# Kernel optimization log

Hardware: AMD Instinct MI355X
Metric: run time of the kernel (lower is better)

Reference implementation:

```python
import jax, jax.numpy as jnp
import numpy as np

B, SQ, SK, D, H = 8, 1024, 1024, 768, 12
HD = D // H  # 64


def setup_inputs() -> dict:
    key = jax.random.key(0)
    ks = jax.random.split(key, 6)
    s = 0.02
    return {
        "hidden_states": jax.random.normal(ks[0], (B, SQ, D), jnp.float32),
        "context": jax.random.normal(ks[1], (B, SK, D), jnp.float32),
        "attention_mask": jnp.zeros((B, 1, 1, SK), jnp.float32),
        "Wq": jax.random.normal(ks[2], (D, D), jnp.float32) * s,
        "bq": jnp.zeros((D,), jnp.float32),
        "Wk": jax.random.normal(ks[3], (D, D), jnp.float32) * s,
        "bk": jnp.zeros((D,), jnp.float32),
        "Wv": jax.random.normal(ks[4], (D, D), jnp.float32) * s,
        "bv": jnp.zeros((D,), jnp.float32),
    }


def _split_heads(x):
    # [B, S, D] -> [B, H, S, HD]
    b, s, _ = x.shape
    return x.reshape(b, s, H, HD).transpose(0, 2, 1, 3)


def reference(hidden_states, context, attention_mask, Wq, bq, Wk, bk, Wv, bv):
    q = _split_heads(hidden_states @ Wq + bq)   # [B,H,SQ,HD]
    k = _split_heads(context @ Wk + bk)         # [B,H,SK,HD]
    v = _split_heads(context @ Wv + bv)         # [B,H,SK,HD]
    scores = jnp.einsum("bhqd,bhkd->bhqk", q, k) / jnp.sqrt(jnp.float32(HD))
    scores = scores + attention_mask            # broadcast [B,1,1,SK]
    probs = jax.nn.softmax(scores, axis=-1)     # dropout p=0 -> identity
    ctx = jnp.einsum("bhqk,bhkd->bhqd", probs, v)
    return ctx.transpose(0, 2, 1, 3).reshape(hidden_states.shape[0], -1, H * HD)
```

## Files before the change

### kernel.cpp

```cpp
#include <hip/hip_runtime.h>
#include <hip/hip_bf16.h>
#include <cstdint>

#define B_  8
#define SQ_ 1024
#define SK_ 1024
#define D_  768
#define H_  12
#define HD_ 64

typedef __attribute__((ext_vector_type(8))) short s16x8;
typedef __attribute__((ext_vector_type(4))) float f32x4;
typedef __attribute__((ext_vector_type(16))) float f32x16;

__device__ __forceinline__ float bf2f(ushort u) {
    union { uint32_t i; float f; } v; v.i = ((uint32_t)u) << 16; return v.f;
}
__device__ __forceinline__ ushort f2bf(float f) {
    __hip_bfloat16 h = __float2bfloat16(f);
    union { __hip_bfloat16 h; ushort u; } v; v.h = h; return v.u;
}
__device__ __forceinline__ uint32_t pk32(float a, float b) {
    return (uint32_t)f2bf(a) | ((uint32_t)f2bf(b) << 16);
}
__device__ __forceinline__ float fexp2(float x) {
#if __has_builtin(__builtin_amdgcn_exp2f)
    return __builtin_amdgcn_exp2f(x);
#else
    return exp2f(x);
#endif
}
__device__ __forceinline__ void xch(uint32_t a, uint32_t b, bool lo, uint32_t& x, uint32_t& y) {
    uint32_t bx = (uint32_t)__shfl_xor((int)b, 32);
    uint32_t ax = (uint32_t)__shfl_xor((int)a, 32);
    x = lo ? a : bx;
    y = lo ? ax : b;
}

__global__ void convX(const float4* __restrict__ src, ushort* __restrict__ dst, int n4) {
    int i = blockIdx.x * blockDim.x + threadIdx.x;
    int stride = gridDim.x * blockDim.x;
    for (; i < n4; i += stride) {
        float4 v = src[i];
        ushort4 o = { f2bf(v.x), f2bf(v.y), f2bf(v.z), f2bf(v.w) };
        *reinterpret_cast<ushort4*>(dst + (size_t)i * 4) = o;
    }
}

__global__ void convWT(const float* __restrict__ W, ushort* __restrict__ WT) {
    __shared__ float t[32][33];
    int k0 = blockIdx.x * 32, n0 = blockIdx.y * 32;
    int tx = threadIdx.x & 31, ty = threadIdx.x >> 5;
#pragma unroll
    for (int rr = 0; rr < 4; ++rr)
        t[ty + 8 * rr][tx] = W[(size_t)(k0 + ty + 8 * rr) * D_ + n0 + tx];
    __syncthreads();
#pragma unroll
    for (int rr = 0; rr < 4; ++rr)
        WT[(size_t)(n0 + ty + 8 * rr) * D_ + k0 + tx] = f2bf(t[tx][ty + 8 * rr]);
}

#define GL16(g, l)                                                                     \
    __builtin_amdgcn_global_load_lds((const __attribute__((address_space(1))) void*)(g), \
                                     (__attribute__((address_space(3))) void*)(l), 16, 0, 0)

__global__ __launch_bounds__(256) void gemm_qkv(
    const ushort* __restrict__ hb, const ushort* __restrict__ cb,
    const ushort* __restrict__ wqt, const ushort* __restrict__ wkt, const ushort* __restrict__ wvt,
    const float* __restrict__ bq, const float* __restrict__ bk, const float* __restrict__ bv,
    ushort* __restrict__ qout, ushort* __restrict__ kout, ushort* __restrict__ vtout)
{
    const int z = blockIdx.z;
    const ushort* A    = (z == 0) ? hb : cb;
    const ushort* Wt   = (z == 0) ? wqt : (z == 1) ? wkt : wvt;
    const float*  bias = (z == 0) ? bq  : (z == 1) ? bk  : bv;

    __shared__ ushort As[128 * 32];
    __shared__ ushort Bs[128 * 32];

    const int tid = threadIdx.x;
    const int w = tid >> 6, l = tid & 63;
    const int g = l >> 4, c = l & 15;
    const int wr = w >> 1, wc = w & 1;
    const int m0 = blockIdx.x * 128;
    const int n0 = blockIdx.y * 128;

    f32x4 acc[4][4];
#pragma unroll
    for (int mi = 0; mi < 4; ++mi)
#pragma unroll
        for (int ni = 0; ni < 4; ++ni) acc[mi][ni] = (f32x4){0.f, 0.f, 0.f, 0.f};

    for (int kt = 0; kt < D_ / 32; ++kt) {
        __syncthreads();
#pragma unroll
        for (int j = 0; j < 2; ++j) {
            int cc = (j * 4 + w) * 64 + l;
            int row = cc >> 2, c8 = cc & 3;
            const ushort* ga = A  + (size_t)(m0 + row) * D_ + kt * 32 + c8 * 8;
            GL16(ga, (char*)As + (size_t)(j * 4 + w) * 1024);
            const ushort* gb = Wt + (size_t)(n0 + row) * D_ + kt * 32 + c8 * 8;
            GL16(gb, (char*)Bs + (size_t)(j * 4 + w) * 1024);
        }
        __syncthreads();

        s16x8 af[4], bfr[4];
#pragma unroll
        for (int mi = 0; mi < 4; ++mi)
            af[mi] = *(const s16x8*)&As[(wr * 64 + mi * 16 + c) * 32 + g * 8];
#pragma unroll
        for (int ni = 0; ni < 4; ++ni)
            bfr[ni] = *(const s16x8*)&Bs[(wc * 64 + ni * 16 + c) * 32 + g * 8];
#pragma unroll
        for (int mi = 0; mi < 4; ++mi)
#pragma unroll
            for (int ni = 0; ni < 4; ++ni)
                acc[mi][ni] = __builtin_amdgcn_mfma_f32_16x16x32_bf16(af[mi], bfr[ni], acc[mi][ni], 0, 0, 0);
    }

    if (z < 2) {
        ushort* Out = (z == 0) ? qout : kout;
#pragma unroll
        for (int ni = 0; ni < 4; ++ni) {
            int ncol = n0 + wc * 64 + ni * 16 + c;
            float bv_ = bias[ncol];
#pragma unroll
            for (int mi = 0; mi < 4; ++mi) {
#pragma unroll
                for (int r = 0; r < 4; ++r) {
                    int mrow = m0 + wr * 64 + mi * 16 + 4 * g + r;
                    Out[(size_t)mrow * D_ + ncol] = f2bf(acc[mi][ni][r] + bv_);
                }
            }
        }
    } else {
#pragma unroll
        for (int ni = 0; ni < 4; ++ni) {
            int ncol = n0 + wc * 64 + ni * 16 + c;
            float bv_ = bias[ncol];
            int hh = ncol >> 6, dd = ncol & 63;
#pragma unroll
            for (int mi = 0; mi < 4; ++mi) {
                int mrow = m0 + wr * 64 + mi * 16 + 4 * g;
                int bb = mrow >> 10, ss = mrow & 1023;
                ushort4 pk;
                pk.x = f2bf(acc[mi][ni][0] + bv_);
                pk.y = f2bf(acc[mi][ni][1] + bv_);
                pk.z = f2bf(acc[mi][ni][2] + bv_);
                pk.w = f2bf(acc[mi][ni][3] + bv_);
                *reinterpret_cast<ushort4*>(vtout + (size_t)((bb * H_ + hh) * HD_ + dd) * SK_ + ss) = pk;
            }
        }
    }
}

#define MFMA32(a, b, c) __builtin_amdgcn_mfma_f32_32x32x16_bf16(a, b, c, 0, 0, 0)

__device__ __forceinline__ void proc_qs(f32x16 sa, float& m_run, float& ps,
                                        f32x16& o0, f32x16& o1,
                                        const s16x8 v0a, const s16x8 v1a,
                                        const s16x8 v0b, const s16x8 v1b,
                                        const int hi, const bool lo)
{
    const float L2E = 1.44269504f;
    float a0 = fmaxf(fmaxf(sa[0], sa[1]), fmaxf(sa[2], sa[3]));
    float a1 = fmaxf(fmaxf(sa[4], sa[5]), fmaxf(sa[6], sa[7]));
    float a2 = fmaxf(fmaxf(sa[8], sa[9]), fmaxf(sa[10], sa[11]));
    float a3 = fmaxf(fmaxf(sa[12], sa[13]), fmaxf(sa[14], sa[15]));
    float pmax = fmaxf(fmaxf(a0, a1), fmaxf(a2, a3));
    if (__any(pmax > m_run + 8.f)) {
        float mf = fmaxf(pmax, __shfl_xor(pmax, 32));
        float mn = fmaxf(m_run, mf);
        float alpha = fexp2((m_run - mn) * L2E);
        m_run = mn; ps *= alpha;
#pragma unroll
        for (int r = 0; r < 16; ++r) {
            float ar = __shfl(alpha, (r & 3) + 8 * (r >> 2) + 4 * hi);
            o0[r] *= ar; o1[r] *= ar;
        }
    }
    float ml = m_run * L2E;
    float p[16];
#pragma unroll
    for (int r = 0; r < 16; ++r) p[r] = fexp2(sa[r] * L2E - ml);
    ps += (((p[0] + p[1]) + (p[2] + p[3])) + ((p[4] + p[5]) + (p[6] + p[7]))) +
          (((p[8] + p[9]) + (p[10] + p[11])) + ((p[12] + p[13]) + (p[14] + p[15])));
    uint32_t cc[8];
#pragma unroll
    for (int j = 0; j < 8; ++j) cc[j] = pk32(p[2 * j], p[2 * j + 1]);
    uint32_t d0, d1, d2, d3, e0, e1, e2, e3;
    xch(cc[0], cc[2], lo, d0, d2);
    xch(cc[1], cc[3], lo, d1, d3);
    xch(cc[4], cc[6], lo, e0, e2);
    xch(cc[5], cc[7], lo, e1, e3);
    union { uint32_t u[4]; s16x8 v; } ua, ub;
    ua.u[0] = d0; ua.u[1] = d1; ua.u[2] = d2; ua.u[3] = d3;
    ub.u[0] = e0; ub.u[1] = e1; ub.u[2] = e2; ub.u[3] = e3;
    o0 = MFMA32(ua.v, v0a, o0);
    o0 = MFMA32(ub.v, v1a, o0);
    o1 = MFMA32(ua.v, v0b, o1);
    o1 = MFMA32(ub.v, v1b, o1);
}

__global__ __launch_bounds__(256, 3) void attn(
    const ushort* __restrict__ Qb, const ushort* __restrict__ Kb, const ushort* __restrict__ VT,
    const float* __restrict__ amask, float* __restrict__ out)
{
    __shared__ ushort Ks[2][64 * 64];
    __shared__ ushort Vs[2][64 * 64];
    __shared__ float  Ms[1024];

    const int tid = threadIdx.x;
    const int w   = tid >> 6;
    const int l   = tid & 63;
    const int hi  = l >> 5;
    const int l31 = l & 31;
    const bool lo = (hi == 0);
    const int swz = (l31 & 7) << 4;
    const int q0w = blockIdx.x * 128 + w * 32;
    const int h = blockIdx.y, b = blockIdx.z;

    ((float4*)Ms)[tid] = ((const float4*)(amask + b * SK_))[tid];

    s16x8 qf[4];
#pragma unroll
    for (int s = 0; s < 4; ++s) {
        const ushort* gq = Qb + (size_t)(b * SQ_ + q0w + l31) * D_ + h * HD_ + s * 16 + hi * 8;
        s16x8 v = *(const s16x8*)gq;
#pragma unroll
        for (int i = 0; i < 8; ++i) v[i] = (short)f2bf(bf2f((ushort)v[i]) * 0.125f);
        qf[s] = v;
    }

    const int row0 = tid >> 3, c8 = tid & 7;
    const int ldsoff = row0 * 128 + ((c8 * 16) ^ ((row0 & 7) << 4));
    const ushort* kp = Kb + (size_t)(b * SK_ + row0) * D_ + h * HD_ + c8 * 8;
    const ushort* vp = VT + (size_t)((b * H_ + h) * HD_ + row0) * SK_ + c8 * 8;

    {
        *(uint4*)((char*)Ks[0] + ldsoff)        = *(const uint4*)(kp);
        *(uint4*)((char*)Ks[0] + ldsoff + 4096) = *(const uint4*)(kp + 32 * D_);
        *(uint4*)((char*)Vs[0] + ldsoff)        = *(const uint4*)(vp);
        *(uint4*)((char*)Vs[0] + ldsoff + 4096) = *(const uint4*)(vp + 32 * SK_);
        kp += 64 * D_; vp += 64;
    }
    __syncthreads();

    f32x16 o[2];
#pragma unroll
    for (int db = 0; db < 2; ++db)
#pragma unroll
        for (int r = 0; r < 16; ++r) o[db][r] = 0.f;
    float m_run = -INFINITY, ps = 0.f;

#define TILE(CUR, NXT, T)                                                              \
    {                                                                                  \
        uint4 nk0 = *(const uint4*)(kp);                                               \
        uint4 nk1 = *(const uint4*)(kp + 32 * D_);                                     \
        uint4 nv0 = *(const uint4*)(vp);                                               \
        uint4 nv1 = *(const uint4*)(vp + 32 * SK_);                                    \
        if ((T) < 14) { kp += 64 * D_; vp += 64; }                                     \
        _Pragma("unroll")                                                              \
        for (int blk = 0; blk < 2; ++blk) {                                            \
            const int kvb = (T) * 64 + blk * 32;                                       \
            union { f32x4 q[4]; f32x16 v; } mku;                                       \
            _Pragma("unroll")                                                          \
            for (int t = 0; t < 4; ++t)                                                \
                mku.q[t] = *(const f32x4*)&Ms[kvb + 4 * hi + 8 * t];                   \
            s16x8 kfr[4];                                                              \
            _Pragma("unroll")                                                          \
            for (int s = 0; s < 4; ++s)                                                \
                kfr[s] = *(const s16x8*)((const char*)Ks[CUR] + (blk * 32 + l31) * 128 \
                                         + ((s * 32 + hi * 16) ^ swz));                \
            s16x8 vfr[2][2];                                                           \
            _Pragma("unroll")                                                          \
            for (int sl = 0; sl < 2; ++sl)                                             \
                _Pragma("unroll")                                                      \
                for (int db = 0; db < 2; ++db)                                         \
                    vfr[sl][db] = *(const s16x8*)((const char*)Vs[CUR] +               \
                        (db * 32 + l31) * 128 + ((blk * 64 + sl * 32 + hi * 16) ^ swz)); \
            f32x16 sa = MFMA32(kfr[0], qf[0], mku.v);                                  \
            sa = MFMA32(kfr[1], qf[1], sa);                                            \
            sa = MFMA32(kfr[2], qf[2], sa);                                            \
            sa = MFMA32(kfr[3], qf[3], sa);                                            \
            proc_qs(sa, m_run, ps, o[0], o[1],                                         \
                    vfr[0][0], vfr[1][0], vfr[0][1], vfr[1][1], hi, lo);               \
        }                                                                              \
        *(uint4*)((char*)Ks[NXT] + ldsoff)        = nk0;                               \
        *(uint4*)((char*)Ks[NXT] + ldsoff + 4096) = nk1;                               \
        *(uint4*)((char*)Vs[NXT] + ldsoff)        = nv0;                               \
        *(uint4*)((char*)Vs[NXT] + ldsoff + 4096) = nv1;                               \
        __syncthreads();                                                               \
    }

    for (int tt = 0; tt < 8; ++tt) {
        TILE(0, 1, 2 * tt)
        TILE(1, 0, 2 * tt + 1)
    }
#undef TILE

    float pf = ps + __shfl_xor(ps, 32);
    float inv = 1.f / pf;
#pragma unroll
    for (int r = 0; r < 16; ++r) {
        int qr = (r & 3) + 8 * (r >> 2) + 4 * hi;
        float iv = __shfl(inv, qr);
        float* op = out + (size_t)(b * SQ_ + q0w + qr) * D_ + h * HD_ + l31;
        op[0]  = o[0][r] * iv;
        op[32] = o[1][r] * iv;
    }
}

extern "C" void kernel_launch(void* const* d_in, const int* in_sizes, int n_in,
                              void* d_out, int out_size, void* d_ws, size_t ws_size,
                              hipStream_t stream) {
    (void)in_sizes; (void)n_in; (void)out_size; (void)ws_size;
    const float* hidden  = (const float*)d_in[0];
    const float* context = (const float*)d_in[1];
    const float* amask   = (const float*)d_in[2];
    const float* Wq = (const float*)d_in[3];
    const float* bq = (const float*)d_in[4];
    const float* Wk = (const float*)d_in[5];
    const float* bk = (const float*)d_in[6];
    const float* Wv = (const float*)d_in[7];
    const float* bv = (const float*)d_in[8];
    float* out = (float*)d_out;

    char* ws = (char*)d_ws;
    ushort* hb  = (ushort*)(ws);
    ushort* cb  = (ushort*)(ws + 12582912);
    ushort* wqt = (ushort*)(ws + 25165824);
    ushort* wkt = (ushort*)(ws + 26345472);
    ushort* wvt = (ushort*)(ws + 27525120);
    ushort* qb  = (ushort*)(ws + 28704768);
    ushort* kb  = (ushort*)(ws + 41287680);
    ushort* vt  = (ushort*)(ws + 53870592);

    int n4 = (B_ * SQ_ * D_) / 4;
    convX<<<2048, 256, 0, stream>>>((const float4*)hidden, hb, n4);
    convX<<<2048, 256, 0, stream>>>((const float4*)context, cb, n4);
    dim3 gw(24, 24);
    convWT<<<gw, 256, 0, stream>>>(Wq, wqt);
    convWT<<<gw, 256, 0, stream>>>(Wk, wkt);
    convWT<<<gw, 256, 0, stream>>>(Wv, wvt);
    gemm_qkv<<<dim3(64, 6, 3), 256, 0, stream>>>(hb, cb, wqt, wkt, wvt, bq, bk, bv, qb, kb, vt);
    attn<<<dim3(8, 12, 8), 256, 0, stream>>>(qb, kb, vt, amask, out);
}
```

Before: 218.7 us.

## Double-buffer QKV GEMM LDS tiles with XOR swizzle and fuse conversion kernels

Merges the five fp32-to-bf16 conversion and weight-transpose launches into one kernel that splits its blocks between the two jobs. The QKV GEMM now uses two LDS buffers so the async global-to-LDS load for the next k-tile overlaps the MFMA work on the current one, with one barrier per iteration. An XOR swizzle on the 16-byte column chunk is meant to reduce LDS bank conflicts on fragment reads. This doubles LDS use per block, which may lower occupancy, and the single barrier relies on the loads having landed by the end of each iteration.

```diff
diff --git a/kernel.cpp b/kernel.cpp
--- a/kernel.cpp
+++ b/kernel.cpp
@@ -37,27 +37,39 @@
     y = lo ? ax : b;
 }
 
-__global__ void convX(const float4* __restrict__ src, ushort* __restrict__ dst, int n4) {
-    int i = blockIdx.x * blockDim.x + threadIdx.x;
-    int stride = gridDim.x * blockDim.x;
-    for (; i < n4; i += stride) {
-        float4 v = src[i];
-        ushort4 o = { f2bf(v.x), f2bf(v.y), f2bf(v.z), f2bf(v.w) };
-        *reinterpret_cast<ushort4*>(dst + (size_t)i * 4) = o;
-    }
-}
-
-__global__ void convWT(const float* __restrict__ W, ushort* __restrict__ WT) {
-    __shared__ float t[32][33];
-    int k0 = blockIdx.x * 32, n0 = blockIdx.y * 32;
-    int tx = threadIdx.x & 31, ty = threadIdx.x >> 5;
-#pragma unroll
-    for (int rr = 0; rr < 4; ++rr)
-        t[ty + 8 * rr][tx] = W[(size_t)(k0 + ty + 8 * rr) * D_ + n0 + tx];
-    __syncthreads();
-#pragma unroll
-    for (int rr = 0; rr < 4; ++rr)
-        WT[(size_t)(n0 + ty + 8 * rr) * D_ + k0 + tx] = f2bf(t[tx][ty + 8 * rr]);
+__global__ void convAll(const float4* __restrict__ hsrc, const float4* __restrict__ csrc,
+                        ushort* __restrict__ hb, ushort* __restrict__ cb,
+                        const float* __restrict__ Wq, const float* __restrict__ Wk,
+                        const float* __restrict__ Wv,
+                        ushort* __restrict__ wqt, ushort* __restrict__ wkt,
+                        ushort* __restrict__ wvt, int n4) {
+    const int bid = blockIdx.x;
+    if (bid < 1728) {
+        __shared__ float t[32][33];
+        const int which = bid / 576, tt = bid % 576;
+        const float* W = (which == 0) ? Wq : (which == 1) ? Wk : Wv;
+        ushort* WT     = (which == 0) ? wqt : (which == 1) ? wkt : wvt;
+        const int k0 = (tt % 24) * 32, n0 = (tt / 24) * 32;
+        const int tx = threadIdx.x & 31, ty = threadIdx.x >> 5;
+#pragma unroll
+        for (int rr = 0; rr < 4; ++rr)
+            t[ty + 8 * rr][tx] = W[(size_t)(k0 + ty + 8 * rr) * D_ + n0 + tx];
+        __syncthreads();
+#pragma unroll
+        for (int rr = 0; rr < 4; ++rr)
+            WT[(size_t)(n0 + ty + 8 * rr) * D_ + k0 + tx] = f2bf(t[tx][ty + 8 * rr]);
+    } else {
+        const int n2 = 2 * n4;
+        int i = (bid - 1728) * 256 + threadIdx.x;
+        const int stride = (gridDim.x - 1728) * 256;
+        for (; i < n2; i += stride) {
+            const bool first = (i < n4);
+            const int ii = first ? i : i - n4;
+            float4 v = first ? hsrc[ii] : csrc[ii];
+            ushort4 o = { f2bf(v.x), f2bf(v.y), f2bf(v.z), f2bf(v.w) };
+            *reinterpret_cast<ushort4*>((first ? hb : cb) + (size_t)ii * 4) = o;
+        }
+    }
 }
 
 #define GL16(g, l)                                                                     \
@@ -75,8 +87,8 @@
     const ushort* Wt   = (z == 0) ? wqt : (z == 1) ? wkt : wvt;
     const float*  bias = (z == 0) ? bq  : (z == 1) ? bk  : bv;
 
-    __shared__ ushort As[128 * 32];
-    __shared__ ushort Bs[128 * 32];
+    __shared__ ushort As[2][128 * 32];
+    __shared__ ushort Bs[2][128 * 32];
 
     const int tid = threadIdx.x;
     const int w = tid >> 6, l = tid & 63;
@@ -84,6 +96,7 @@
     const int wr = w >> 1, wc = w & 1;
     const int m0 = blockIdx.x * 128;
     const int n0 = blockIdx.y * 128;
+    const int c3 = c & 3;
 
     f32x4 acc[4][4];
 #pragma unroll
@@ -91,32 +104,46 @@
 #pragma unroll
         for (int ni = 0; ni < 4; ++ni) acc[mi][ni] = (f32x4){0.f, 0.f, 0.f, 0.f};
 
+#define STAGE(BUF, KT)                                                                 \
+    {                                                                                  \
+        _Pragma("unroll")                                                              \
+        for (int j = 0; j < 2; ++j) {                                                  \
+            int cc = (j * 4 + w) * 64 + l;                                             \
+            int row = cc >> 2;                                                         \
+            int gc = (cc & 3) ^ (row & 3);                                             \
+            GL16(A  + (size_t)(m0 + row) * D_ + (KT) * 32 + gc * 8,                    \
+                 (char*)As[BUF] + (size_t)(j * 4 + w) * 1024);                         \
+            GL16(Wt + (size_t)(n0 + row) * D_ + (KT) * 32 + gc * 8,                    \
+                 (char*)Bs[BUF] + (size_t)(j * 4 + w) * 1024);                         \
+        }                                                                              \
+    }
+
+    STAGE(0, 0)
+    __syncthreads();
+
+    int cur = 0;
     for (int kt = 0; kt < D_ / 32; ++kt) {
-        __syncthreads();
-#pragma unroll
-        for (int j = 0; j < 2; ++j) {
-            int cc = (j * 4 + w) * 64 + l;
-            int row = cc >> 2, c8 = cc & 3;
-            const ushort* ga = A  + (size_t)(m0 + row) * D_ + kt * 32 + c8 * 8;
-            GL16(ga, (char*)As + (size_t)(j * 4 + w) * 1024);
-            const ushort* gb = Wt + (size_t)(n0 + row) * D_ + kt * 32 + c8 * 8;
-            GL16(gb, (char*)Bs + (size_t)(j * 4 + w) * 1024);
-        }
-        __syncthreads();
+        if (kt < D_ / 32 - 1) STAGE(cur ^ 1, kt + 1)
 
         s16x8 af[4], bfr[4];
 #pragma unroll
         for (int mi = 0; mi < 4; ++mi)
-            af[mi] = *(const s16x8*)&As[(wr * 64 + mi * 16 + c) * 32 + g * 8];
+            af[mi] = *(const s16x8*)((const char*)As[cur] +
+                                     (wr * 64 + mi * 16 + c) * 64 + ((g ^ c3) << 4));
 #pragma unroll
         for (int ni = 0; ni < 4; ++ni)
-            bfr[ni] = *(const s16x8*)&Bs[(wc * 64 + ni * 16 + c) * 32 + g * 8];
+            bfr[ni] = *(const s16x8*)((const char*)Bs[cur] +
+                                      (wc * 64 + ni * 16 + c) * 64 + ((g ^ c3) << 4));
 #pragma unroll
         for (int mi = 0; mi < 4; ++mi)
 #pragma unroll
             for (int ni = 0; ni < 4; ++ni)
                 acc[mi][ni] = __builtin_amdgcn_mfma_f32_16x16x32_bf16(af[mi], bfr[ni], acc[mi][ni], 0, 0, 0);
-    }
+
+        __syncthreads();
+        cur ^= 1;
+    }
+#undef STAGE
 
     if (z < 2) {
         ushort* Out = (z == 0) ? qout : kout;
@@ -337,12 +364,8 @@
     ushort* vt  = (ushort*)(ws + 53870592);
 
     int n4 = (B_ * SQ_ * D_) / 4;
-    convX<<<2048, 256, 0, stream>>>((const float4*)hidden, hb, n4);
-    convX<<<2048, 256, 0, stream>>>((const float4*)context, cb, n4);
-    dim3 gw(24, 24);
-    convWT<<<gw, 256, 0, stream>>>(Wq, wqt);
-    convWT<<<gw, 256, 0, stream>>>(Wk, wkt);
-    convWT<<<gw, 256, 0, stream>>>(Wv, wvt);
+    convAll<<<1728 + 2048, 256, 0, stream>>>((const float4*)hidden, (const float4*)context,
+                                             hb, cb, Wq, Wk, Wv, wqt, wkt, wvt, n4);
     gemm_qkv<<<dim3(64, 6, 3), 256, 0, stream>>>(hb, cb, wqt, wkt, wvt, bq, bk, bv, qb, kb, vt);
     attn<<<dim3(8, 12, 8), 256, 0, stream>>>(qb, kb, vt, amask, out);
 }
```

New measurement: 216.4 us. No clear change (-1.0%).
